# Kernel tuning notes

Hardware: AMD Instinct MI355X
Metric: run time of the kernel (lower is better)

The kernel has to match this reference:

```python
import jax, jax.numpy as jnp
import numpy as np

N, E = 50000, 600000
H, ED = 128, 64
LN_EPS = 1e-5


def _ln(x, g, b):
    mu = jnp.mean(x, axis=-1, keepdims=True)
    var = jnp.mean(jnp.square(x - mu), axis=-1, keepdims=True)
    return (x - mu) * jax.lax.rsqrt(var + LN_EPS) * g + b


def setup_inputs() -> dict:
    key = jax.random.key(0)
    ks = jax.random.split(key, 20)
    p = lambda k, shp: (jax.random.normal(k, shp, dtype=jnp.float32) * 0.02)
    return {
        "x": jax.random.normal(ks[0], (N, H), dtype=jnp.float32),
        "edge_src": jax.random.randint(ks[1], (E,), 0, N, dtype=jnp.int32),
        "edge_dst": jax.random.randint(ks[2], (E,), 0, N, dtype=jnp.int32),
        "edge_emb": jax.random.normal(ks[3], (E, ED), dtype=jnp.float32),
        "ln1_g": jnp.ones((H,), jnp.float32), "ln1_b": jnp.zeros((H,), jnp.float32),
        "W_self": p(ks[4], (H, H)), "b_self": jnp.zeros((H,), jnp.float32),
        "W_m1": p(ks[5], (H + ED, H)), "b_m1": jnp.zeros((H,), jnp.float32),
        "W_m2": p(ks[6], (H, H)), "b_m2": jnp.zeros((H,), jnp.float32),
        "W_g1": p(ks[7], (2 * H + ED, H)), "b_g1": jnp.zeros((H,), jnp.float32),
        "W_g2": p(ks[8], (H, 1)), "b_g2": jnp.zeros((1,), jnp.float32),
        "W_agg": p(ks[9], (H, H)), "b_agg": jnp.zeros((H,), jnp.float32),
        "ln2_g": jnp.ones((H,), jnp.float32), "ln2_b": jnp.zeros((H,), jnp.float32),
        "W_f1": p(ks[10], (H, 2 * H)), "b_f1": jnp.zeros((2 * H,), jnp.float32),
        "W_f2": p(ks[11], (2 * H, H)), "b_f2": jnp.zeros((H,), jnp.float32),
    }


def reference(x, edge_src, edge_dst, edge_emb,
              ln1_g, ln1_b, W_self, b_self,
              W_m1, b_m1, W_m2, b_m2,
              W_g1, b_g1, W_g2, b_g2,
              W_agg, b_agg, ln2_g, ln2_b,
              W_f1, b_f1, W_f2, b_f2):
    n = x.shape[0]
    h = _ln(x, ln1_g, ln1_b)                      # [N,H]
    hs = h[edge_src]                              # [E,H] gather
    hd = h[edge_dst]                              # [E,H] gather
    # message MLP on [h_src || e]
    m_in = jnp.concatenate([hs, edge_emb], axis=-1)            # [E,H+ED]
    msg = jax.nn.gelu(m_in @ W_m1 + b_m1, approximate=False) @ W_m2 + b_m2
    # gate MLP on [h_dst || h_src || e]
    g_in = jnp.concatenate([hd, hs, edge_emb], axis=-1)        # [E,2H+ED]
    gate = jax.nn.sigmoid(jax.nn.gelu(g_in @ W_g1 + b_g1, approximate=False) @ W_g2 + b_g2)
    edge_repr = gate * msg                                     # [E,H]
    # scatter-mean aggregate to destination nodes
    agg = jax.ops.segment_sum(edge_repr, edge_dst, num_segments=n)   # [N,H]
    deg = jax.ops.segment_sum(jnp.ones((edge_dst.shape[0], 1), x.dtype),
                              edge_dst, num_segments=n)              # [N,1]
    agg = agg / jnp.maximum(deg, 1.0)
    update = (h @ W_self + b_self) + (agg @ W_agg + b_agg)
    out = x + update                                           # residual
    ffn_in = _ln(out, ln2_g, ln2_b)
    ffn_up = jax.nn.gelu(ffn_in @ W_f1 + b_f1, approximate=False) @ W_f2 + b_f2
    out = out + ffn_up                                         # residual
    return (out, edge_repr)
```

## Files before the change

### kernel.cpp

```cpp
#include <hip/hip_runtime.h>
#include <math.h>

#define N_NODES 50000
#define N_EDGES 600000
#define NTILES (N_EDGES / 64)

typedef __attribute__((ext_vector_type(8))) short bf16x8;
typedef __attribute__((ext_vector_type(4))) float f32x4;

__device__ __forceinline__ unsigned short f2bf(float f){
  union { float f; unsigned int u; } v; v.f = f;
  unsigned int u = v.u;
  unsigned int r = (u + 0x7fffu + ((u >> 16) & 1u)) >> 16;
  return (unsigned short)r;
}
__device__ __forceinline__ float gelu_f(float x){
  return 0.5f * x * (1.0f + erff(x * 0.70710678118654752440f));
}

__global__ void pack_kernel(const float* __restrict__ W, unsigned short* __restrict__ out,
                            int K, int N){
  int id = blockIdx.x * 256 + threadIdx.x;
  if (id >= K * N) return;
  int j = id & 7;
  int q = (id >> 3) & 3;
  int rest = id >> 5;
  int n = rest % N;
  int kt = rest / N;
  int k = kt * 32 + q * 8 + j;
  out[id] = f2bf(W[(size_t)k * N + n]);
}

__global__ __launch_bounds__(256) void ln1_kernel(const float* __restrict__ x,
                                                  const float* __restrict__ g,
                                                  const float* __restrict__ b,
                                                  unsigned short* __restrict__ h_bf, int n){
  int row = blockIdx.x * 4 + (threadIdx.x >> 6);
  if (row >= n) return;
  int lane = threadIdx.x & 63;
  const float* xr = x + (size_t)row * 128;
  float2 v = *(const float2*)(xr + lane * 2);
  float s = v.x + v.y;
  float s2 = v.x * v.x + v.y * v.y;
#pragma unroll
  for (int off = 32; off; off >>= 1){ s += __shfl_xor(s, off); s2 += __shfl_xor(s2, off); }
  float mu = s * (1.f / 128.f);
  float var = s2 * (1.f / 128.f) - mu * mu;
  float rs = rsqrtf(var + 1e-5f);
  int c = lane * 2;
  ushort2 o;
  o.x = f2bf((v.x - mu) * rs * g[c] + b[c]);
  o.y = f2bf((v.y - mu) * rs * g[c + 1] + b[c + 1]);
  *(ushort2*)(h_bf + (size_t)row * 128 + c) = o;
}

__global__ __launch_bounds__(256, 2) void edge_kernel(
    const unsigned short* __restrict__ h_bf,
    const int* __restrict__ esrc, const int* __restrict__ edst,
    const float* __restrict__ emb,
    const unsigned short* __restrict__ Wm1p, const float* __restrict__ bm1,
    const unsigned short* __restrict__ Wm2p, const float* __restrict__ bm2,
    const unsigned short* __restrict__ Wg1p, const float* __restrict__ bg1,
    const float* __restrict__ wg2, const float* __restrict__ bg2,
    float* __restrict__ out_e, float* __restrict__ agg, float* __restrict__ deg)
{
  __shared__ unsigned short smA[64][328];
  __shared__ unsigned short smT[64][136];
  __shared__ float smGP[4][64];
  __shared__ float smGate[64];
  __shared__ int smDst[64];

  const int t = threadIdx.x;
  const int wave = t >> 6, lane = t & 63;
  const int q = lane >> 4, ln = lane & 15;
  const int kq = q * 8;

  bf16x8 wg[10][2], w1[6][2], w2[4][2];
  float bg1r[2], wg2r[2], bm1r[2], bm2r[2];
#pragma unroll
  for (int j = 0; j < 2; j++){
    const int col = wave * 32 + j * 16 + ln;
    bg1r[j] = bg1[col]; wg2r[j] = wg2[col]; bm1r[j] = bm1[col]; bm2r[j] = bm2[col];
#pragma unroll
    for (int kt = 0; kt < 10; kt++) wg[kt][j] = *(const bf16x8*)(Wg1p + (((size_t)kt * 128 + col) * 4 + q) * 8);
#pragma unroll
    for (int kt = 0; kt < 6; kt++)  w1[kt][j] = *(const bf16x8*)(Wm1p + (((size_t)kt * 128 + col) * 4 + q) * 8);
#pragma unroll
    for (int kt = 0; kt < 4; kt++)  w2[kt][j] = *(const bf16x8*)(Wm2p + (((size_t)kt * 128 + col) * 4 + q) * 8);
  }
  const float bg2v = bg2[0];
  const int r4 = t >> 2, i4 = t & 3;

  for (int tile = blockIdx.x; tile < NTILES; tile += gridDim.x){
    const int e0 = tile * 64;
    __syncthreads();

    {
      const int e = e0 + r4;
      const int ds = edst[e], ss = esrc[e];
      if (i4 == 0){ smDst[r4] = ds; atomicAdd(&deg[ds], 1.0f); }
      const uint4* hdp = (const uint4*)(h_bf + (size_t)ds * 128 + i4 * 32);
      const uint4* hsp = (const uint4*)(h_bf + (size_t)ss * 128 + i4 * 32);
      uint4* a0 = (uint4*)&smA[r4][i4 * 32];
      uint4* a1 = (uint4*)&smA[r4][128 + i4 * 32];
#pragma unroll
      for (int k2 = 0; k2 < 4; k2++){ a0[k2] = hdp[k2]; a1[k2] = hsp[k2]; }
      const float4* ep = (const float4*)(emb + (size_t)e * 64 + i4 * 16);
#pragma unroll
      for (int k2 = 0; k2 < 4; k2++){
        float4 f = ep[k2];
        ushort4 u; u.x = f2bf(f.x); u.y = f2bf(f.y); u.z = f2bf(f.z); u.w = f2bf(f.w);
        *(ushort4*)&smA[r4][256 + i4 * 16 + k2 * 4] = u;
      }
    }
    __syncthreads();

    {
      f32x4 acc[4][2];
#pragma unroll
      for (int rt = 0; rt < 4; rt++)
#pragma unroll
        for (int j = 0; j < 2; j++) acc[rt][j] = (f32x4){0.f, 0.f, 0.f, 0.f};
#pragma unroll
      for (int kt = 0; kt < 10; kt++){
        bf16x8 a[4];
#pragma unroll
        for (int rt = 0; rt < 4; rt++) a[rt] = *(const bf16x8*)&smA[rt * 16 + ln][kt * 32 + kq];
#pragma unroll
        for (int rt = 0; rt < 4; rt++)
#pragma unroll
          for (int j = 0; j < 2; j++)
            acc[rt][j] = __builtin_amdgcn_mfma_f32_16x16x32_bf16(a[rt], wg[kt][j], acc[rt][j], 0, 0, 0);
      }
      float p[4][4];
#pragma unroll
      for (int rt = 0; rt < 4; rt++)
#pragma unroll
        for (int r = 0; r < 4; r++)
          p[rt][r] = gelu_f(acc[rt][0][r] + bg1r[0]) * wg2r[0]
                   + gelu_f(acc[rt][1][r] + bg1r[1]) * wg2r[1];
#pragma unroll
      for (int m = 1; m < 16; m <<= 1){
#pragma unroll
        for (int rt = 0; rt < 4; rt++)
#pragma unroll
          for (int r = 0; r < 4; r++) p[rt][r] += __shfl_xor(p[rt][r], m);
      }
      if (ln == 0){
#pragma unroll
        for (int rt = 0; rt < 4; rt++)
#pragma unroll
          for (int r = 0; r < 4; r++) smGP[wave][rt * 16 + q * 4 + r] = p[rt][r];
      }
    }
    __syncthreads();
    if (t < 64)
      smGate[t] = 1.f / (1.f + expf(-(smGP[0][t] + smGP[1][t] + smGP[2][t] + smGP[3][t] + bg2v)));

    {
      f32x4 acc[4][2];
#pragma unroll
      for (int rt = 0; rt < 4; rt++)
#pragma unroll
        for (int j = 0; j < 2; j++) acc[rt][j] = (f32x4){0.f, 0.f, 0.f, 0.f};
#pragma unroll
      for (int kt = 0; kt < 6; kt++){
        bf16x8 a[4];
#pragma unroll
        for (int rt = 0; rt < 4; rt++) a[rt] = *(const bf16x8*)&smA[rt * 16 + ln][128 + kt * 32 + kq];
#pragma unroll
        for (int rt = 0; rt < 4; rt++)
#pragma unroll
          for (int j = 0; j < 2; j++)
            acc[rt][j] = __builtin_amdgcn_mfma_f32_16x16x32_bf16(a[rt], w1[kt][j], acc[rt][j], 0, 0, 0);
      }
#pragma unroll
      for (int rt = 0; rt < 4; rt++)
#pragma unroll
        for (int j = 0; j < 2; j++){
          const int col = wave * 32 + j * 16 + ln;
          const float bia = bm1r[j];
#pragma unroll
          for (int r = 0; r < 4; r++)
            smT[rt * 16 + q * 4 + r][col] = f2bf(gelu_f(acc[rt][j][r] + bia));
        }
    }
    __syncthreads();

    {
      f32x4 acc[4][2];
#pragma unroll
      for (int rt = 0; rt < 4; rt++)
#pragma unroll
        for (int j = 0; j < 2; j++) acc[rt][j] = (f32x4){0.f, 0.f, 0.f, 0.f};
#pragma unroll
      for (int kt = 0; kt < 4; kt++){
        bf16x8 a[4];
#pragma unroll
        for (int rt = 0; rt < 4; rt++) a[rt] = *(const bf16x8*)&smT[rt * 16 + ln][kt * 32 + kq];
#pragma unroll
        for (int rt = 0; rt < 4; rt++)
#pragma unroll
          for (int j = 0; j < 2; j++)
            acc[rt][j] = __builtin_amdgcn_mfma_f32_16x16x32_bf16(a[rt], w2[kt][j], acc[rt][j], 0, 0, 0);
      }
#pragma unroll
      for (int rt = 0; rt < 4; rt++)
#pragma unroll
        for (int j = 0; j < 2; j++){
          const int col = wave * 32 + j * 16 + ln;
          const float bia = bm2r[j];
#pragma unroll
          for (int r = 0; r < 4; r++){
            const int row = rt * 16 + q * 4 + r;
            const float val = smGate[row] * (acc[rt][j][r] + bia);
            out_e[(size_t)(e0 + row) * 128 + col] = val;
            atomicAdd(&agg[(size_t)smDst[row] * 128 + col], val);
          }
        }
    }
  }
}

__global__ __launch_bounds__(256, 2) void node_kernel(
    const float* __restrict__ x, const unsigned short* __restrict__ h_bf,
    const float* __restrict__ agg, const float* __restrict__ deg,
    const unsigned short* __restrict__ Wselfp, const float* __restrict__ bself,
    const unsigned short* __restrict__ Waggp, const float* __restrict__ bagg,
    const float* __restrict__ ln2g, const float* __restrict__ ln2b,
    const unsigned short* __restrict__ Wf1p, const float* __restrict__ bf1,
    const unsigned short* __restrict__ Wf2p, const float* __restrict__ bf2,
    float* __restrict__ out, int n)
{
  __shared__ unsigned short smH[32][136];
  __shared__ unsigned short smG[32][136];
  __shared__ float smO[32][132];
  __shared__ unsigned short smU[32][264];

  const int t = threadIdx.x;
  const int n0 = blockIdx.x * 32;

  {
    const int r = t >> 3, i = t & 7;
    int gr = n0 + r; if (gr >= n) gr = n - 1;
    const uint4* hp = (const uint4*)(h_bf + (size_t)gr * 128 + i * 16);
    uint4* dp = (uint4*)&smH[r][i * 16];
    dp[0] = hp[0]; dp[1] = hp[1];
    float sc = 1.f / fmaxf(deg[gr], 1.f);
    const float4* ap = (const float4*)(agg + (size_t)gr * 128 + i * 16);
#pragma unroll
    for (int k2 = 0; k2 < 4; k2++){
      float4 f = ap[k2];
      ushort4 u; u.x = f2bf(f.x * sc); u.y = f2bf(f.y * sc); u.z = f2bf(f.z * sc); u.w = f2bf(f.w * sc);
      *(ushort4*)&smG[r][i * 16 + k2 * 4] = u;
    }
  }
  __syncthreads();

  const int wave = t >> 6, lane = t & 63;
  const int q = lane >> 4, ln = lane & 15;
  const int mtile = wave >> 1;
  const int cg = wave & 1;
  const int arow = mtile * 16 + ln;
  const int kq = q * 8;

  f32x4 acc[4];
#pragma unroll
  for (int i = 0; i < 4; i++) acc[i] = (f32x4){0.f, 0.f, 0.f, 0.f};
#pragma unroll
  for (int kt = 0; kt < 4; kt++){
    bf16x8 a = *(const bf16x8*)&smH[arow][kt * 32 + kq];
#pragma unroll
    for (int j = 0; j < 4; j++){
      int col = (cg * 4 + j) * 16 + ln;
      bf16x8 b = *(const bf16x8*)(Wselfp + (((size_t)kt * 128 + col) * 4 + q) * 8);
      acc[j] = __builtin_amdgcn_mfma_f32_16x16x32_bf16(a, b, acc[j], 0, 0, 0);
    }
  }
#pragma unroll
  for (int kt = 0; kt < 4; kt++){
    bf16x8 a = *(const bf16x8*)&smG[arow][kt * 32 + kq];
#pragma unroll
    for (int j = 0; j < 4; j++){
      int col = (cg * 4 + j) * 16 + ln;
      bf16x8 b = *(const bf16x8*)(Waggp + (((size_t)kt * 128 + col) * 4 + q) * 8);
      acc[j] = __builtin_amdgcn_mfma_f32_16x16x32_bf16(a, b, acc[j], 0, 0, 0);
    }
  }
#pragma unroll
  for (int j = 0; j < 4; j++){
    int col = (cg * 4 + j) * 16 + ln;
    float bia = bself[col] + bagg[col];
#pragma unroll
    for (int r = 0; r < 4; r++){
      int row = mtile * 16 + q * 4 + r;
      int gr = n0 + row; if (gr >= n) gr = n - 1;
      smO[row][col] = x[(size_t)gr * 128 + col] + acc[j][r] + bia;
    }
  }
  __syncthreads();

  {
    const int r = t >> 3, i = t & 7;
    float v[16];
    float s = 0.f, s2 = 0.f;
    const float4* op = (const float4*)&smO[r][i * 16];
#pragma unroll
    for (int k2 = 0; k2 < 4; k2++){
      float4 f = op[k2];
      v[k2 * 4 + 0] = f.x; v[k2 * 4 + 1] = f.y; v[k2 * 4 + 2] = f.z; v[k2 * 4 + 3] = f.w;
      s += f.x + f.y + f.z + f.w;
      s2 += f.x * f.x + f.y * f.y + f.z * f.z + f.w * f.w;
    }
#pragma unroll
    for (int m = 1; m < 8; m <<= 1){ s += __shfl_xor(s, m); s2 += __shfl_xor(s2, m); }
    float mu = s * (1.f / 128.f);
    float var = s2 * (1.f / 128.f) - mu * mu;
    float rs = rsqrtf(var + 1e-5f);
#pragma unroll
    for (int c2 = 0; c2 < 16; c2++){
      int col = i * 16 + c2;
      smH[r][col] = f2bf((v[c2] - mu) * rs * ln2g[col] + ln2b[col]);
    }
  }
  __syncthreads();

  {
    f32x4 au[8];
#pragma unroll
    for (int i = 0; i < 8; i++) au[i] = (f32x4){0.f, 0.f, 0.f, 0.f};
#pragma unroll
    for (int kt = 0; kt < 4; kt++){
      bf16x8 a = *(const bf16x8*)&smH[arow][kt * 32 + kq];
#pragma unroll
      for (int j = 0; j < 8; j++){
        int col = (cg * 8 + j) * 16 + ln;
        bf16x8 b = *(const bf16x8*)(Wf1p + (((size_t)kt * 256 + col) * 4 + q) * 8);
        au[j] = __builtin_amdgcn_mfma_f32_16x16x32_bf16(a, b, au[j], 0, 0, 0);
      }
    }
#pragma unroll
    for (int j = 0; j < 8; j++){
      int col = (cg * 8 + j) * 16 + ln;
      float bia = bf1[col];
#pragma unroll
      for (int r = 0; r < 4; r++){
        smU[mtile * 16 + q * 4 + r][col] = f2bf(gelu_f(au[j][r] + bia));
      }
    }
  }
  __syncthreads();

  {
    f32x4 a2[4];
#pragma unroll
    for (int i = 0; i < 4; i++) a2[i] = (f32x4){0.f, 0.f, 0.f, 0.f};
#pragma unroll
    for (int kt = 0; kt < 8; kt++){
      bf16x8 a = *(const bf16x8*)&smU[arow][kt * 32 + kq];
#pragma unroll
      for (int j = 0; j < 4; j++){
        int col = (cg * 4 + j) * 16 + ln;
        bf16x8 b = *(const bf16x8*)(Wf2p + (((size_t)kt * 128 + col) * 4 + q) * 8);
        a2[j] = __builtin_amdgcn_mfma_f32_16x16x32_bf16(a, b, a2[j], 0, 0, 0);
      }
    }
#pragma unroll
    for (int j = 0; j < 4; j++){
      int col = (cg * 4 + j) * 16 + ln;
      float bia = bf2[col];
#pragma unroll
      for (int r = 0; r < 4; r++){
        int row = mtile * 16 + q * 4 + r;
        int gr = n0 + row;
        if (gr < n) out[(size_t)gr * 128 + col] = smO[row][col] + a2[j][r] + bia;
      }
    }
  }
}

extern "C" void kernel_launch(void* const* d_in, const int* in_sizes, int n_in,
                              void* d_out, int out_size, void* d_ws, size_t ws_size,
                              hipStream_t stream){
  const float* x     = (const float*)d_in[0];
  const int*   esrc  = (const int*)d_in[1];
  const int*   edst  = (const int*)d_in[2];
  const float* eemb  = (const float*)d_in[3];
  const float* ln1g  = (const float*)d_in[4];
  const float* ln1b  = (const float*)d_in[5];
  const float* Wself = (const float*)d_in[6];
  const float* bself = (const float*)d_in[7];
  const float* Wm1   = (const float*)d_in[8];
  const float* bm1   = (const float*)d_in[9];
  const float* Wm2   = (const float*)d_in[10];
  const float* bm2   = (const float*)d_in[11];
  const float* Wg1   = (const float*)d_in[12];
  const float* bg1   = (const float*)d_in[13];
  const float* wg2   = (const float*)d_in[14];
  const float* bg2   = (const float*)d_in[15];
  const float* Wagg  = (const float*)d_in[16];
  const float* bagg  = (const float*)d_in[17];
  const float* ln2g  = (const float*)d_in[18];
  const float* ln2b  = (const float*)d_in[19];
  const float* Wf1   = (const float*)d_in[20];
  const float* bf1   = (const float*)d_in[21];
  const float* Wf2   = (const float*)d_in[22];
  const float* bf2   = (const float*)d_in[23];

  char* ws = (char*)d_ws;
  float* agg = (float*)(ws + 0);
  float* deg = (float*)(ws + 25600000);
  unsigned short* h_bf = (unsigned short*)(ws + 25800000);
  unsigned short* Wselfp = (unsigned short*)(ws + 38600000);
  unsigned short* Wm1p  = Wselfp + 16384;
  unsigned short* Wm2p  = Wm1p + 24576;
  unsigned short* Wg1p  = Wm2p + 16384;
  unsigned short* Waggp = Wg1p + 40960;
  unsigned short* Wf1p  = Waggp + 16384;
  unsigned short* Wf2p  = Wf1p + 32768;

  hipMemsetAsync(agg, 0, 25600000 + 200000, stream);

  pack_kernel<<<64, 256, 0, stream>>>(Wself, Wselfp, 128, 128);
  pack_kernel<<<96, 256, 0, stream>>>(Wm1, Wm1p, 192, 128);
  pack_kernel<<<64, 256, 0, stream>>>(Wm2, Wm2p, 128, 128);
  pack_kernel<<<160, 256, 0, stream>>>(Wg1, Wg1p, 320, 128);
  pack_kernel<<<64, 256, 0, stream>>>(Wagg, Waggp, 128, 128);
  pack_kernel<<<128, 256, 0, stream>>>(Wf1, Wf1p, 128, 256);
  pack_kernel<<<128, 256, 0, stream>>>(Wf2, Wf2p, 256, 128);

  ln1_kernel<<<12500, 256, 0, stream>>>(x, ln1g, ln1b, h_bf, N_NODES);

  float* out_nodes = (float*)d_out;
  float* out_edges = out_nodes + (size_t)N_NODES * 128;

  edge_kernel<<<512, 256, 0, stream>>>(h_bf, esrc, edst, eemb,
      Wm1p, bm1, Wm2p, bm2, Wg1p, bg1, wg2, bg2, out_edges, agg, deg);

  node_kernel<<<(N_NODES + 31) / 32, 256, 0, stream>>>(x, h_bf, agg, deg,
      Wselfp, bself, Waggp, bagg, ln2g, ln2b, Wf1p, bf1, Wf2p, bf2, out_nodes, N_NODES);
}
```

Before: 953.7 us.

## Prefetch next edge tile, fuse gate/message GEMMs, make node kernel persistent

The edge kernel now register-prefetches the next tile's gathered node rows and edge embeddings while computing the current tile. It also fuses the gate and message-MLP first-layer GEMMs into one K loop that shares the A fragments, using transposed MFMA operands so results can be written to LDS as vectors. It drops one block barrier by computing the gate per wave. The node kernel becomes a persistent grid of 768 blocks that keeps all weights in registers instead of reloading them per tile, with vectorized bias and output handling. This raises register pressure and could cost occupancy.

New measurement: 1.026 ms. 1.08x slower.

```diff
diff --git a/kernel.cpp b/kernel.cpp
--- a/kernel.cpp
+++ b/kernel.cpp
@@ -4,6 +4,7 @@
 #define N_NODES 50000
 #define N_EDGES 600000
 #define NTILES (N_EDGES / 64)
+#define NODE_TILES ((N_NODES + 31) / 32)
 
 typedef __attribute__((ext_vector_type(8))) short bf16x8;
 typedef __attribute__((ext_vector_type(4))) float f32x4;
@@ -64,10 +65,10 @@
     const float* __restrict__ wg2, const float* __restrict__ bg2,
     float* __restrict__ out_e, float* __restrict__ agg, float* __restrict__ deg)
 {
-  __shared__ unsigned short smA[64][328];
-  __shared__ unsigned short smT[64][136];
-  __shared__ float smGP[4][64];
-  __shared__ float smGate[64];
+  __shared__ __align__(16) unsigned short smA[64][328];
+  __shared__ __align__(16) unsigned short smT[64][136];
+  __shared__ __align__(16) float smGP[4][64];
+  __shared__ __align__(16) float smGateW[4][64];
   __shared__ int smDst[64];
 
   const int t = threadIdx.x;
@@ -76,11 +77,13 @@
   const int kq = q * 8;
 
   bf16x8 wg[10][2], w1[6][2], w2[4][2];
-  float bg1r[2], wg2r[2], bm1r[2], bm2r[2];
+  float bg1r[2], wg2r[2], bm2r[2];
+  float4 bm1t[2];
 #pragma unroll
   for (int j = 0; j < 2; j++){
     const int col = wave * 32 + j * 16 + ln;
-    bg1r[j] = bg1[col]; wg2r[j] = wg2[col]; bm1r[j] = bm1[col]; bm2r[j] = bm2[col];
+    bg1r[j] = bg1[col]; wg2r[j] = wg2[col]; bm2r[j] = bm2[col];
+    bm1t[j] = *(const float4*)(bm1 + wave * 32 + j * 16 + q * 4);
 #pragma unroll
     for (int kt = 0; kt < 10; kt++) wg[kt][j] = *(const bf16x8*)(Wg1p + (((size_t)kt * 128 + col) * 4 + q) * 8);
 #pragma unroll
@@ -91,24 +94,35 @@
   const float bg2v = bg2[0];
   const int r4 = t >> 2, i4 = t & 3;
 
+  uint4 hdR[4], hsR[4];
+  float4 emR[4];
+  int dstR;
+  {
+    const int e = blockIdx.x * 64 + r4;
+    dstR = edst[e];
+    const int ss = esrc[e];
+    const uint4* hdp = (const uint4*)(h_bf + (size_t)dstR * 128 + i4 * 32);
+    const uint4* hsp = (const uint4*)(h_bf + (size_t)ss * 128 + i4 * 32);
+#pragma unroll
+    for (int k2 = 0; k2 < 4; k2++){ hdR[k2] = hdp[k2]; hsR[k2] = hsp[k2]; }
+    const float4* ep = (const float4*)(emb + (size_t)e * 64 + i4 * 16);
+#pragma unroll
+    for (int k2 = 0; k2 < 4; k2++) emR[k2] = ep[k2];
+  }
+
   for (int tile = blockIdx.x; tile < NTILES; tile += gridDim.x){
     const int e0 = tile * 64;
     __syncthreads();
 
     {
-      const int e = e0 + r4;
-      const int ds = edst[e], ss = esrc[e];
-      if (i4 == 0){ smDst[r4] = ds; atomicAdd(&deg[ds], 1.0f); }
-      const uint4* hdp = (const uint4*)(h_bf + (size_t)ds * 128 + i4 * 32);
-      const uint4* hsp = (const uint4*)(h_bf + (size_t)ss * 128 + i4 * 32);
+      if (i4 == 0){ smDst[r4] = dstR; atomicAdd(&deg[dstR], 1.0f); }
       uint4* a0 = (uint4*)&smA[r4][i4 * 32];
       uint4* a1 = (uint4*)&smA[r4][128 + i4 * 32];
 #pragma unroll
-      for (int k2 = 0; k2 < 4; k2++){ a0[k2] = hdp[k2]; a1[k2] = hsp[k2]; }
-      const float4* ep = (const float4*)(emb + (size_t)e * 64 + i4 * 16);
+      for (int k2 = 0; k2 < 4; k2++){ a0[k2] = hdR[k2]; a1[k2] = hsR[k2]; }
 #pragma unroll
       for (int k2 = 0; k2 < 4; k2++){
-        float4 f = ep[k2];
+        float4 f = emR[k2];
         ushort4 u; u.x = f2bf(f.x); u.y = f2bf(f.y); u.z = f2bf(f.z); u.w = f2bf(f.w);
         *(ushort4*)&smA[r4][256 + i4 * 16 + k2 * 4] = u;
       }
@@ -116,13 +130,31 @@
     __syncthreads();
 
     {
-      f32x4 acc[4][2];
+      const int tn = tile + gridDim.x;
+      const int eb = (tn < NTILES) ? tn * 64 : e0;
+      const int e = eb + r4;
+      dstR = edst[e];
+      const int ss = esrc[e];
+      const uint4* hdp = (const uint4*)(h_bf + (size_t)dstR * 128 + i4 * 32);
+      const uint4* hsp = (const uint4*)(h_bf + (size_t)ss * 128 + i4 * 32);
+#pragma unroll
+      for (int k2 = 0; k2 < 4; k2++){ hdR[k2] = hdp[k2]; hsR[k2] = hsp[k2]; }
+      const float4* ep = (const float4*)(emb + (size_t)e * 64 + i4 * 16);
+#pragma unroll
+      for (int k2 = 0; k2 < 4; k2++) emR[k2] = ep[k2];
+    }
+
+    {
+      f32x4 accg[4][2], accm[4][2];
 #pragma unroll
       for (int rt = 0; rt < 4; rt++)
 #pragma unroll
-        for (int j = 0; j < 2; j++) acc[rt][j] = (f32x4){0.f, 0.f, 0.f, 0.f};
-#pragma unroll
-      for (int kt = 0; kt < 10; kt++){
+        for (int j = 0; j < 2; j++){
+          accg[rt][j] = (f32x4){0.f, 0.f, 0.f, 0.f};
+          accm[rt][j] = (f32x4){0.f, 0.f, 0.f, 0.f};
+        }
+#pragma unroll
+      for (int kt = 0; kt < 4; kt++){
         bf16x8 a[4];
 #pragma unroll
         for (int rt = 0; rt < 4; rt++) a[rt] = *(const bf16x8*)&smA[rt * 16 + ln][kt * 32 + kq];
@@ -130,39 +162,8 @@
         for (int rt = 0; rt < 4; rt++)
 #pragma unroll
           for (int j = 0; j < 2; j++)
-            acc[rt][j] = __builtin_amdgcn_mfma_f32_16x16x32_bf16(a[rt], wg[kt][j], acc[rt][j], 0, 0, 0);
-      }
-      float p[4][4];
-#pragma unroll
-      for (int rt = 0; rt < 4; rt++)
-#pragma unroll
-        for (int r = 0; r < 4; r++)
-          p[rt][r] = gelu_f(acc[rt][0][r] + bg1r[0]) * wg2r[0]
-                   + gelu_f(acc[rt][1][r] + bg1r[1]) * wg2r[1];
-#pragma unroll
-      for (int m = 1; m < 16; m <<= 1){
-#pragma unroll
-        for (int rt = 0; rt < 4; rt++)
-#pragma unroll
-          for (int r = 0; r < 4; r++) p[rt][r] += __shfl_xor(p[rt][r], m);
-      }
-      if (ln == 0){
-#pragma unroll
-        for (int rt = 0; rt < 4; rt++)
-#pragma unroll
-          for (int r = 0; r < 4; r++) smGP[wave][rt * 16 + q * 4 + r] = p[rt][r];
-      }
-    }
-    __syncthreads();
-    if (t < 64)
-      smGate[t] = 1.f / (1.f + expf(-(smGP[0][t] + smGP[1][t] + smGP[2][t] + smGP[3][t] + bg2v)));
-
-    {
-      f32x4 acc[4][2];
-#pragma unroll
-      for (int rt = 0; rt < 4; rt++)
-#pragma unroll
-        for (int j = 0; j < 2; j++) acc[rt][j] = (f32x4){0.f, 0.f, 0.f, 0.f};
+            accg[rt][j] = __builtin_amdgcn_mfma_f32_16x16x32_bf16(a[rt], wg[kt][j], accg[rt][j], 0, 0, 0);
+      }
 #pragma unroll
       for (int kt = 0; kt < 6; kt++){
         bf16x8 a[4];
@@ -171,23 +172,55 @@
 #pragma unroll
         for (int rt = 0; rt < 4; rt++)
 #pragma unroll
-          for (int j = 0; j < 2; j++)
-            acc[rt][j] = __builtin_amdgcn_mfma_f32_16x16x32_bf16(a[rt], w1[kt][j], acc[rt][j], 0, 0, 0);
-      }
+          for (int j = 0; j < 2; j++){
+            accg[rt][j] = __builtin_amdgcn_mfma_f32_16x16x32_bf16(a[rt], wg[kt + 4][j], accg[rt][j], 0, 0, 0);
+            accm[rt][j] = __builtin_amdgcn_mfma_f32_16x16x32_bf16(w1[kt][j], a[rt], accm[rt][j], 0, 0, 0);
+          }
+      }
+      float p[4][4];
 #pragma unroll
       for (int rt = 0; rt < 4; rt++)
 #pragma unroll
+        for (int r = 0; r < 4; r++)
+          p[rt][r] = gelu_f(accg[rt][0][r] + bg1r[0]) * wg2r[0]
+                   + gelu_f(accg[rt][1][r] + bg1r[1]) * wg2r[1];
+#pragma unroll
+      for (int m = 1; m < 16; m <<= 1){
+#pragma unroll
+        for (int rt = 0; rt < 4; rt++)
+#pragma unroll
+          for (int r = 0; r < 4; r++) p[rt][r] += __shfl_xor(p[rt][r], m);
+      }
+      if (ln == 0){
+#pragma unroll
+        for (int rt = 0; rt < 4; rt++)
+#pragma unroll
+          for (int r = 0; r < 4; r++) smGP[wave][rt * 16 + q * 4 + r] = p[rt][r];
+      }
+#pragma unroll
+      for (int rt = 0; rt < 4; rt++)
+#pragma unroll
         for (int j = 0; j < 2; j++){
-          const int col = wave * 32 + j * 16 + ln;
-          const float bia = bm1r[j];
-#pragma unroll
-          for (int r = 0; r < 4; r++)
-            smT[rt * 16 + q * 4 + r][col] = f2bf(gelu_f(acc[rt][j][r] + bia));
-        }
-    }
-    __syncthreads();
-
-    {
+          ushort4 u;
+          u.x = f2bf(gelu_f(accm[rt][j][0] + bm1t[j].x));
+          u.y = f2bf(gelu_f(accm[rt][j][1] + bm1t[j].y));
+          u.z = f2bf(gelu_f(accm[rt][j][2] + bm1t[j].z));
+          u.w = f2bf(gelu_f(accm[rt][j][3] + bm1t[j].w));
+          *(ushort4*)&smT[rt * 16 + ln][wave * 32 + j * 16 + q * 4] = u;
+        }
+    }
+    __syncthreads();
+
+    {
+      float sgp = smGP[0][lane] + smGP[1][lane] + smGP[2][lane] + smGP[3][lane] + bg2v;
+      smGateW[wave][lane] = 1.f / (1.f + expf(-sgp));
+    }
+    __builtin_amdgcn_wave_barrier();
+
+    {
+      float4 gv4[4];
+#pragma unroll
+      for (int rt = 0; rt < 4; rt++) gv4[rt] = *(const float4*)&smGateW[wave][rt * 16 + q * 4];
       f32x4 acc[4][2];
 #pragma unroll
       for (int rt = 0; rt < 4; rt++)
@@ -213,7 +246,7 @@
 #pragma unroll
           for (int r = 0; r < 4; r++){
             const int row = rt * 16 + q * 4 + r;
-            const float val = smGate[row] * (acc[rt][j][r] + bia);
+            const float val = gv4[rt][r] * (acc[rt][j][r] + bia);
             out_e[(size_t)(e0 + row) * 128 + col] = val;
             atomicAdd(&agg[(size_t)smDst[row] * 128 + col], val);
           }
@@ -222,7 +255,7 @@
   }
 }
 
-__global__ __launch_bounds__(256, 2) void node_kernel(
+__global__ __launch_bounds__(256, 3) void node_kernel(
     const float* __restrict__ x, const unsigned short* __restrict__ h_bf,
     const float* __restrict__ agg, const float* __restrict__ deg,
     const unsigned short* __restrict__ Wselfp, const float* __restrict__ bself,
@@ -232,148 +265,200 @@
     const unsigned short* __restrict__ Wf2p, const float* __restrict__ bf2,
     float* __restrict__ out, int n)
 {
-  __shared__ unsigned short smH[32][136];
-  __shared__ unsigned short smG[32][136];
-  __shared__ float smO[32][132];
-  __shared__ unsigned short smU[32][264];
+  __shared__ __align__(16) unsigned short smH[32][136];
+  __shared__ __align__(16) unsigned short smG[32][136];
+  __shared__ __align__(16) float smO[32][132];
+  __shared__ __align__(16) unsigned short smU[32][264];
 
   const int t = threadIdx.x;
-  const int n0 = blockIdx.x * 32;
-
-  {
-    const int r = t >> 3, i = t & 7;
-    int gr = n0 + r; if (gr >= n) gr = n - 1;
-    const uint4* hp = (const uint4*)(h_bf + (size_t)gr * 128 + i * 16);
-    uint4* dp = (uint4*)&smH[r][i * 16];
-    dp[0] = hp[0]; dp[1] = hp[1];
-    float sc = 1.f / fmaxf(deg[gr], 1.f);
-    const float4* ap = (const float4*)(agg + (size_t)gr * 128 + i * 16);
-#pragma unroll
-    for (int k2 = 0; k2 < 4; k2++){
-      float4 f = ap[k2];
-      ushort4 u; u.x = f2bf(f.x * sc); u.y = f2bf(f.y * sc); u.z = f2bf(f.z * sc); u.w = f2bf(f.w * sc);
-      *(ushort4*)&smG[r][i * 16 + k2 * 4] = u;
-    }
-  }
-  __syncthreads();
-
   const int wave = t >> 6, lane = t & 63;
   const int q = lane >> 4, ln = lane & 15;
-  const int mtile = wave >> 1;
-  const int cg = wave & 1;
-  const int arow = mtile * 16 + ln;
   const int kq = q * 8;
 
-  f32x4 acc[4];
-#pragma unroll
-  for (int i = 0; i < 4; i++) acc[i] = (f32x4){0.f, 0.f, 0.f, 0.f};
-#pragma unroll
-  for (int kt = 0; kt < 4; kt++){
-    bf16x8 a = *(const bf16x8*)&smH[arow][kt * 32 + kq];
-#pragma unroll
-    for (int j = 0; j < 4; j++){
-      int col = (cg * 4 + j) * 16 + ln;
-      bf16x8 b = *(const bf16x8*)(Wselfp + (((size_t)kt * 128 + col) * 4 + q) * 8);
-      acc[j] = __builtin_amdgcn_mfma_f32_16x16x32_bf16(a, b, acc[j], 0, 0, 0);
-    }
+  bf16x8 ws[4][2], wa[4][2], w1f[4][4], w2f[8][2];
+  float4 bsat[2], bf1t[4], bf2t[2];
+#pragma unroll
+  for (int j = 0; j < 2; j++){
+    const int col = wave * 32 + j * 16 + ln;
+#pragma unroll
+    for (int kt = 0; kt < 4; kt++){
+      ws[kt][j] = *(const bf16x8*)(Wselfp + (((size_t)kt * 128 + col) * 4 + q) * 8);
+      wa[kt][j] = *(const bf16x8*)(Waggp  + (((size_t)kt * 128 + col) * 4 + q) * 8);
+    }
+#pragma unroll
+    for (int kt = 0; kt < 8; kt++)
+      w2f[kt][j] = *(const bf16x8*)(Wf2p + (((size_t)kt * 128 + col) * 4 + q) * 8);
+    const int cb = wave * 32 + j * 16 + q * 4;
+    float4 b1 = *(const float4*)(bself + cb);
+    float4 b2 = *(const float4*)(bagg + cb);
+    bsat[j].x = b1.x + b2.x; bsat[j].y = b1.y + b2.y;
+    bsat[j].z = b1.z + b2.z; bsat[j].w = b1.w + b2.w;
+    bf2t[j] = *(const float4*)(bf2 + cb);
   }
 #pragma unroll
-  for (int kt = 0; kt < 4; kt++){
-    bf16x8 a = *(const bf16x8*)&smG[arow][kt * 32 + kq];
-#pragma unroll
-    for (int j = 0; j < 4; j++){
-      int col = (cg * 4 + j) * 16 + ln;
-      bf16x8 b = *(const bf16x8*)(Waggp + (((size_t)kt * 128 + col) * 4 + q) * 8);
-      acc[j] = __builtin_amdgcn_mfma_f32_16x16x32_bf16(a, b, acc[j], 0, 0, 0);
-    }
+  for (int j = 0; j < 4; j++){
+    const int col = wave * 64 + j * 16 + ln;
+#pragma unroll
+    for (int kt = 0; kt < 4; kt++)
+      w1f[kt][j] = *(const bf16x8*)(Wf1p + (((size_t)kt * 256 + col) * 4 + q) * 8);
+    bf1t[j] = *(const float4*)(bf1 + wave * 64 + j * 16 + q * 4);
   }
-#pragma unroll
-  for (int j = 0; j < 4; j++){
-    int col = (cg * 4 + j) * 16 + ln;
-    float bia = bself[col] + bagg[col];
-#pragma unroll
-    for (int r = 0; r < 4; r++){
-      int row = mtile * 16 + q * 4 + r;
-      int gr = n0 + row; if (gr >= n) gr = n - 1;
-      smO[row][col] = x[(size_t)gr * 128 + col] + acc[j][r] + bia;
-    }
-  }
-  __syncthreads();
-
-  {
-    const int r = t >> 3, i = t & 7;
-    float v[16];
-    float s = 0.f, s2 = 0.f;
-    const float4* op = (const float4*)&smO[r][i * 16];
-#pragma unroll
-    for (int k2 = 0; k2 < 4; k2++){
-      float4 f = op[k2];
-      v[k2 * 4 + 0] = f.x; v[k2 * 4 + 1] = f.y; v[k2 * 4 + 2] = f.z; v[k2 * 4 + 3] = f.w;
-      s += f.x + f.y + f.z + f.w;
-      s2 += f.x * f.x + f.y * f.y + f.z * f.z + f.w * f.w;
-    }
-#pragma unroll
-    for (int m = 1; m < 8; m <<= 1){ s += __shfl_xor(s, m); s2 += __shfl_xor(s2, m); }
-    float mu = s * (1.f / 128.f);
-    float var = s2 * (1.f / 128.f) - mu * mu;
-    float rs = rsqrtf(var + 1e-5f);
-#pragma unroll
-    for (int c2 = 0; c2 < 16; c2++){
-      int col = i * 16 + c2;
-      smH[r][col] = f2bf((v[c2] - mu) * rs * ln2g[col] + ln2b[col]);
-    }
-  }
-  __syncthreads();
-
-  {
-    f32x4 au[8];
-#pragma unroll
-    for (int i = 0; i < 8; i++) au[i] = (f32x4){0.f, 0.f, 0.f, 0.f};
-#pragma unroll
-    for (int kt = 0; kt < 4; kt++){
-      bf16x8 a = *(const bf16x8*)&smH[arow][kt * 32 + kq];
-#pragma unroll
-      for (int j = 0; j < 8; j++){
-        int col = (cg * 8 + j) * 16 + ln;
-        bf16x8 b = *(const bf16x8*)(Wf1p + (((size_t)kt * 256 + col) * 4 + q) * 8);
-        au[j] = __builtin_amdgcn_mfma_f32_16x16x32_bf16(a, b, au[j], 0, 0, 0);
-      }
-    }
-#pragma unroll
-    for (int j = 0; j < 8; j++){
-      int col = (cg * 8 + j) * 16 + ln;
-      float bia = bf1[col];
-#pragma unroll
-      for (int r = 0; r < 4; r++){
-        smU[mtile * 16 + q * 4 + r][col] = f2bf(gelu_f(au[j][r] + bia));
-      }
-    }
-  }
-  __syncthreads();
-
-  {
-    f32x4 a2[4];
-#pragma unroll
-    for (int i = 0; i < 4; i++) a2[i] = (f32x4){0.f, 0.f, 0.f, 0.f};
-#pragma unroll
-    for (int kt = 0; kt < 8; kt++){
-      bf16x8 a = *(const bf16x8*)&smU[arow][kt * 32 + kq];
-#pragma unroll
-      for (int j = 0; j < 4; j++){
-        int col = (cg * 4 + j) * 16 + ln;
-        bf16x8 b = *(const bf16x8*)(Wf2p + (((size_t)kt * 128 + col) * 4 + q) * 8);
-        a2[j] = __builtin_amdgcn_mfma_f32_16x16x32_bf16(a, b, a2[j], 0, 0, 0);
-      }
-    }
-#pragma unroll
-    for (int j = 0; j < 4; j++){
-      int col = (cg * 4 + j) * 16 + ln;
-      float bia = bf2[col];
-#pragma unroll
-      for (int r = 0; r < 4; r++){
-        int row = mtile * 16 + q * 4 + r;
-        int gr = n0 + row;
-        if (gr < n) out[(size_t)gr * 128 + col] = smO[row][col] + a2[j][r] + bia;
+
+  const int r8 = t >> 3, i8 = t & 7;
+
+  for (int tile = blockIdx.x; tile < NODE_TILES; tile += gridDim.x){
+    const int n0 = tile * 32;
+    __syncthreads();
+
+    {
+      int gr = n0 + r8; if (gr >= n) gr = n - 1;
+      const uint4* hp = (const uint4*)(h_bf + (size_t)gr * 128 + i8 * 16);
+      uint4* dp = (uint4*)&smH[r8][i8 * 16];
+      dp[0] = hp[0]; dp[1] = hp[1];
+      float sc = 1.f / fmaxf(deg[gr], 1.f);
+      const float4* ap = (const float4*)(agg + (size_t)gr * 128 + i8 * 16);
+#pragma unroll
+      for (int k2 = 0; k2 < 4; k2++){
+        float4 f = ap[k2];
+        ushort4 u; u.x = f2bf(f.x * sc); u.y = f2bf(f.y * sc); u.z = f2bf(f.z * sc); u.w = f2bf(f.w * sc);
+        *(ushort4*)&smG[r8][i8 * 16 + k2 * 4] = u;
+      }
+    }
+    __syncthreads();
+
+    {
+      f32x4 acc[2][2];
+#pragma unroll
+      for (int rt = 0; rt < 2; rt++)
+#pragma unroll
+        for (int j = 0; j < 2; j++) acc[rt][j] = (f32x4){0.f, 0.f, 0.f, 0.f};
+#pragma unroll
+      for (int kt = 0; kt < 4; kt++){
+        bf16x8 a[2], g[2];
+#pragma unroll
+        for (int rt = 0; rt < 2; rt++){
+          a[rt] = *(const bf16x8*)&smH[rt * 16 + ln][kt * 32 + kq];
+          g[rt] = *(const bf16x8*)&smG[rt * 16 + ln][kt * 32 + kq];
+        }
+#pragma unroll
+        for (int rt = 0; rt < 2; rt++)
+#pragma unroll
+          for (int j = 0; j < 2; j++){
+            acc[rt][j] = __builtin_amdgcn_mfma_f32_16x16x32_bf16(ws[kt][j], a[rt], acc[rt][j], 0, 0, 0);
+            acc[rt][j] = __builtin_amdgcn_mfma_f32_16x16x32_bf16(wa[kt][j], g[rt], acc[rt][j], 0, 0, 0);
+          }
+      }
+#pragma unroll
+      for (int rt = 0; rt < 2; rt++){
+        const int row = rt * 16 + ln;
+        int gr = n0 + row; if (gr >= n) gr = n - 1;
+#pragma unroll
+        for (int j = 0; j < 2; j++){
+          const int cb = wave * 32 + j * 16 + q * 4;
+          const float4 xv = *(const float4*)(x + (size_t)gr * 128 + cb);
+          float4 o;
+          o.x = xv.x + acc[rt][j][0] + bsat[j].x;
+          o.y = xv.y + acc[rt][j][1] + bsat[j].y;
+          o.z = xv.z + acc[rt][j][2] + bsat[j].z;
+          o.w = xv.w + acc[rt][j][3] + bsat[j].w;
+          *(float4*)&smO[row][cb] = o;
+        }
+      }
+    }
+    __syncthreads();
+
+    {
+      float v[16];
+      float s = 0.f, s2 = 0.f;
+      const float4* op = (const float4*)&smO[r8][i8 * 16];
+#pragma unroll
+      for (int k2 = 0; k2 < 4; k2++){
+        float4 f = op[k2];
+        v[k2 * 4 + 0] = f.x; v[k2 * 4 + 1] = f.y; v[k2 * 4 + 2] = f.z; v[k2 * 4 + 3] = f.w;
+        s += f.x + f.y + f.z + f.w;
+        s2 += f.x * f.x + f.y * f.y + f.z * f.z + f.w * f.w;
+      }
+#pragma unroll
+      for (int m = 1; m < 8; m <<= 1){ s += __shfl_xor(s, m); s2 += __shfl_xor(s2, m); }
+      float mu = s * (1.f / 128.f);
+      float var = s2 * (1.f / 128.f) - mu * mu;
+      float rs = rsqrtf(var + 1e-5f);
+#pragma unroll
+      for (int c2 = 0; c2 < 16; c2++){
+        int col = i8 * 16 + c2;
+        smH[r8][col] = f2bf((v[c2] - mu) * rs * ln2g[col] + ln2b[col]);
+      }
+    }
+    __syncthreads();
+
+    {
+      f32x4 au[2][4];
+#pragma unroll
+      for (int rt = 0; rt < 2; rt++)
+#pragma unroll
+        for (int j = 0; j < 4; j++) au[rt][j] = (f32x4){0.f, 0.f, 0.f, 0.f};
+#pragma unroll
+      for (int kt = 0; kt < 4; kt++){
+        bf16x8 a[2];
+#pragma unroll
+        for (int rt = 0; rt < 2; rt++) a[rt] = *(const bf16x8*)&smH[rt * 16 + ln][kt * 32 + kq];
+#pragma unroll
+        for (int rt = 0; rt < 2; rt++)
+#pragma unroll
+          for (int j = 0; j < 4; j++)
+            au[rt][j] = __builtin_amdgcn_mfma_f32_16x16x32_bf16(w1f[kt][j], a[rt], au[rt][j], 0, 0, 0);
+      }
+#pragma unroll
+      for (int rt = 0; rt < 2; rt++){
+        const int row = rt * 16 + ln;
+#pragma unroll
+        for (int j = 0; j < 4; j++){
+          const int cb = wave * 64 + j * 16 + q * 4;
+          ushort4 u;
+          u.x = f2bf(gelu_f(au[rt][j][0] + bf1t[j].x));
+          u.y = f2bf(gelu_f(au[rt][j][1] + bf1t[j].y));
+          u.z = f2bf(gelu_f(au[rt][j][2] + bf1t[j].z));
+          u.w = f2bf(gelu_f(au[rt][j][3] + bf1t[j].w));
+          *(ushort4*)&smU[row][cb] = u;
+        }
+      }
+    }
+    __syncthreads();
+
+    {
+      f32x4 a2[2][2];
+#pragma unroll
+      for (int rt = 0; rt < 2; rt++)
+#pragma unroll
+        for (int j = 0; j < 2; j++) a2[rt][j] = (f32x4){0.f, 0.f, 0.f, 0.f};
+#pragma unroll
+      for (int kt = 0; kt < 8; kt++){
+        bf16x8 a[2];
+#pragma unroll
+        for (int rt = 0; rt < 2; rt++) a[rt] = *(const bf16x8*)&smU[rt * 16 + ln][kt * 32 + kq];
+#pragma unroll
+        for (int rt = 0; rt < 2; rt++)
+#pragma unroll
+          for (int j = 0; j < 2; j++)
+            a2[rt][j] = __builtin_amdgcn_mfma_f32_16x16x32_bf16(w2f[kt][j], a[rt], a2[rt][j], 0, 0, 0);
+      }
+#pragma unroll
+      for (int rt = 0; rt < 2; rt++){
+        const int row = rt * 16 + ln;
+        const int gr = n0 + row;
+        if (gr < n){
+#pragma unroll
+          for (int j = 0; j < 2; j++){
+            const int cb = wave * 32 + j * 16 + q * 4;
+            const float4 ov = *(const float4*)&smO[row][cb];
+            float4 o;
+            o.x = ov.x + a2[rt][j][0] + bf2t[j].x;
+            o.y = ov.y + a2[rt][j][1] + bf2t[j].y;
+            o.z = ov.z + a2[rt][j][2] + bf2t[j].z;
+            o.w = ov.w + a2[rt][j][3] + bf2t[j].w;
+            *(float4*)(out + (size_t)gr * 128 + cb) = o;
+          }
+        }
       }
     }
   }
@@ -437,6 +522,6 @@
   edge_kernel<<<512, 256, 0, stream>>>(h_bf, esrc, edst, eemb,
       Wm1p, bm1, Wm2p, bm2, Wg1p, bg1, wg2, bg2, out_edges, agg, deg);
 
-  node_kernel<<<(N_NODES + 31) / 32, 256, 0, stream>>>(x, h_bf, agg, deg,
+  node_kernel<<<768, 256, 0, stream>>>(x, h_bf, agg, deg,
       Wselfp, bself, Waggp, bagg, ln2g, ln2b, Wf1p, bf1, Wf2p, bf2, out_nodes, N_NODES);
 }
```
